# Kernel tuning notes

Hardware: AMD Instinct MI355X
Metric: run time of the kernel (lower is better)

Reference implementation:

```python
import jax, jax.numpy as jnp
import numpy as np

B = 32          # graphs per batch
NPG = 128       # nodes per graph
EPG = NPG * NPG # edges per graph (dense graph assumption in edge_delete_adap)
C = 64          # in_channels
EPS = 1e-6


def setup_inputs() -> dict:
    key = jax.random.key(0)
    k1, k2, k3, k4 = jax.random.split(key, 4)
    N = B * NPG
    x = jax.random.normal(k1, (N, C), jnp.float32)
    # dense per-graph edges, grouped contiguously by graph (required by the
    # reshape to [B, EPG] inside edge_delete_adap)
    a = jnp.arange(EPG, dtype=jnp.int32)
    src = a // NPG
    dst = a % NPG
    offs = (jnp.arange(B, dtype=jnp.int32) * NPG)[:, None]
    edge_index = jnp.stack([
        (src[None, :] + offs).reshape(-1),
        (dst[None, :] + offs).reshape(-1),
    ])  # [2, B*EPG] int32
    batch = jnp.repeat(jnp.arange(B, dtype=jnp.int32), NPG)  # node -> graph id
    W = jax.random.normal(k2, (2 * C, 1), jnp.float32) / np.sqrt(2 * C).astype(np.float32)
    b = jnp.zeros((1,), jnp.float32)
    rate1 = jax.random.uniform(k3, (B, EPG), jnp.float32)
    rate2 = jax.random.uniform(k4, (B, EPG), jnp.float32)
    return {"x": x, "edge_index": edge_index, "batch": batch,
            "W": W, "b": b, "rate1": rate1, "rate2": rate2}


def _edge_delete_adap(score_flat, rate, nodes):
    # score_flat: [B*EPG]; rate: [B, EPG]
    Bg, E = rate.shape
    s = score_flat.reshape(Bg, E)
    mn = jnp.min(s, axis=1, keepdims=True)
    mx = jnp.max(s, axis=1, keepdims=True)
    s = (s - mn) / (mx - mn + EPS)                  # per-graph min/max normalize
    mask = rate > (1.0 - s)                          # stochastic edge keep
    row = jnp.arange(Bg, dtype=jnp.int32)[:, None]
    col = jnp.arange(E, dtype=jnp.int32)[None, :]
    # index arithmetic from the original nonzero-based selection, computed for
    # ALL positions (padded form); mask marks which columns torch.nonzero keeps.
    idx0 = col // nodes + row * nodes
    idx1 = col % nodes + row * nodes
    new_edge_index = jnp.stack([idx0.reshape(-1), idx1.reshape(-1)])  # [2, B*E]
    return new_edge_index, mask.reshape(-1), s


def reference(x, edge_index, batch, W, b, rate1, rate2):
    # gather + concat edge endpoint features: [E_total, 2C] (dominant traffic)
    feat = jnp.concatenate([x[edge_index[0]], x[edge_index[1]]], axis=-1)
    raw = jax.nn.relu(feat @ W + b)                 # [E_total, 1]; dropout p=0.0
    score = jax.nn.sigmoid(raw).reshape(-1)         # [E_total]
    ei1, m1, s1 = _edge_delete_adap(score, rate1, NPG)
    ei2, m2, s2 = _edge_delete_adap(score, rate2, NPG)
    # original returns (new_edge_index1, new_edge_index2, batch, new_edge_score);
    # dynamic-shape nonzero outputs are returned in padded form + boolean mask.
    return ei1, m1, ei2, m2, batch, s1
```

## Files before the change

### kernel.cpp

```cpp
#include <hip/hip_runtime.h>
#include <math.h>

#define BGRAPH 32
#define NPG    128
#define EPG    (NPG * NPG)
#define CCH    64
#define ETOT   (BGRAPH * EPG)
#define NTOT   (BGRAPH * NPG)

__global__ __launch_bounds__(NPG) void node_kernel(
    const float* __restrict__ x,
    const float* __restrict__ W,
    const float* __restrict__ b,
    double* __restrict__ u,
    double* __restrict__ v,
    double* __restrict__ g_mn,
    double* __restrict__ g_den,
    float* __restrict__ out_batch)
{
    const int g = blockIdx.x;
    const int t = threadIdx.x;
    const int n = g * NPG + t;

    const float* xp = x + (size_t)n * CCH;
    double su = 0.0, sv = 0.0;
    #pragma unroll
    for (int c = 0; c < CCH; ++c) {
        double xc = (double)xp[c];
        su += xc * (double)W[c];
        sv += xc * (double)W[CCH + c];
    }
    const double uu = su + (double)b[0];
    u[n] = uu;
    v[n] = sv;
    out_batch[n] = (float)g;

    __shared__ double r0[NPG], r1[NPG], r2[NPG], r3[NPG];
    r0[t] = uu;
    r1[t] = uu;
    r2[t] = sv;
    r3[t] = sv;
    __syncthreads();
    for (int s = NPG / 2; s > 0; s >>= 1) {
        if (t < s) {
            r0[t] = fmin(r0[t], r0[t + s]);
            r1[t] = fmax(r1[t], r1[t + s]);
            r2[t] = fmin(r2[t], r2[t + s]);
            r3[t] = fmax(r3[t], r3[t + s]);
        }
        __syncthreads();
    }
    if (t == 0) {
        double tmin = r0[0] + r2[0];
        double tmax = r1[0] + r3[0];
        double rmin = tmin > 0.0 ? tmin : 0.0;
        double rmax = tmax > 0.0 ? tmax : 0.0;
        double smn = 1.0 / (1.0 + exp(-rmin));
        double smx = 1.0 / (1.0 + exp(-rmax));
        g_mn[g]  = smn;
        g_den[g] = smx - smn + 1e-6;
    }
}

__global__ __launch_bounds__(256) void edge_kernel(
    const double* __restrict__ u,
    const double* __restrict__ v,
    const double* __restrict__ g_mn,
    const double* __restrict__ g_den,
    const float* __restrict__ rate1,
    const float* __restrict__ rate2,
    float* __restrict__ out)
{
    const int tid = blockIdx.x * blockDim.x + threadIdx.x;
    const int idx = tid << 2;
    const int g   = idx >> 14;
    const int e   = idx & (EPG - 1);
    const int i   = e >> 7;
    const int j0  = e & 127;

    const double uu  = u[g * NPG + i];
    const double mn  = g_mn[g];
    const double den = g_den[g];
    const double* vp = v + g * NPG + j0;

    float4 r1 = *(const float4*)(rate1 + idx);
    float4 r2 = *(const float4*)(rate2 + idx);
    float r1a[4] = {r1.x, r1.y, r1.z, r1.w};
    float r2a[4] = {r2.x, r2.y, r2.z, r2.w};

    float sa[4], m1a[4], m2a[4], i1a[4];
    #pragma unroll
    for (int k = 0; k < 4; ++k) {
        double t   = uu + vp[k];
        double raw = t > 0.0 ? t : 0.0;
        double sig = 1.0 / (1.0 + exp(-raw));
        double s   = (sig - mn) / den;
        double thr = 1.0 - s;
        m1a[k] = ((double)r1a[k] > thr) ? 1.0f : 0.0f;
        m2a[k] = ((double)r2a[k] > thr) ? 1.0f : 0.0f;
        sa[k]  = (float)s;
        i1a[k] = (float)(j0 + k + g * NPG);
    }
    const float i0f = (float)(i + g * NPG);
    float4 i0v = make_float4(i0f, i0f, i0f, i0f);
    float4 i1v = make_float4(i1a[0], i1a[1], i1a[2], i1a[3]);
    float4 m1v = make_float4(m1a[0], m1a[1], m1a[2], m1a[3]);
    float4 m2v = make_float4(m2a[0], m2a[1], m2a[2], m2a[3]);
    float4 sv  = make_float4(sa[0],  sa[1],  sa[2],  sa[3]);

    *(float4*)(out + 0 * (size_t)ETOT + idx) = i0v;
    *(float4*)(out + 1 * (size_t)ETOT + idx) = i1v;
    *(float4*)(out + 2 * (size_t)ETOT + idx) = m1v;
    *(float4*)(out + 3 * (size_t)ETOT + idx) = i0v;
    *(float4*)(out + 4 * (size_t)ETOT + idx) = i1v;
    *(float4*)(out + 5 * (size_t)ETOT + idx) = m2v;
    *(float4*)(out + 6 * (size_t)ETOT + NTOT + idx) = sv;
}

extern "C" void kernel_launch(void* const* d_in, const int* in_sizes, int n_in,
                              void* d_out, int out_size, void* d_ws, size_t ws_size,
                              hipStream_t stream) {
    const float* x     = (const float*)d_in[0];
    const float* W     = (const float*)d_in[3];
    const float* b     = (const float*)d_in[4];
    const float* rate1 = (const float*)d_in[5];
    const float* rate2 = (const float*)d_in[6];
    float* out = (float*)d_out;

    double* u    = (double*)d_ws;
    double* v    = u + NTOT;
    double* gmn  = v + NTOT;
    double* gden = gmn + BGRAPH;

    float* out_batch = out + 6 * (size_t)ETOT;

    node_kernel<<<BGRAPH, NPG, 0, stream>>>(x, W, b, u, v, gmn, gden, out_batch);
    edge_kernel<<<ETOT / 4 / 256, 256, 0, stream>>>(u, v, gmn, gden, rate1, rate2, out);
}
```

Measured before the change: 78.34 us.

## Fuse node projection and edge scoring into one kernel with shared-memory node values

Merges the node and edge kernels into a single launch. Each of the 512 blocks recomputes its graph's node projections (u, v) and the per-graph min/max into shared memory, then scores its 1024 edges. This removes the second launch, the global-memory round trip for u/v/min/max, and the dependency between the two kernels. In exchange, each graph's node work is done 16 times redundantly, which adds x reads and a reduction before the edge work can start in every block. The x loads now use float4.

```diff
diff --git a/kernel.cpp b/kernel.cpp
--- a/kernel.cpp
+++ b/kernel.cpp
@@ -8,80 +8,80 @@
 #define ETOT   (BGRAPH * EPG)
 #define NTOT   (BGRAPH * NPG)
 
-__global__ __launch_bounds__(NPG) void node_kernel(
+__global__ __launch_bounds__(256) void fused_kernel(
     const float* __restrict__ x,
     const float* __restrict__ W,
     const float* __restrict__ b,
-    double* __restrict__ u,
-    double* __restrict__ v,
-    double* __restrict__ g_mn,
-    double* __restrict__ g_den,
-    float* __restrict__ out_batch)
+    const float* __restrict__ rate1,
+    const float* __restrict__ rate2,
+    float* __restrict__ out)
 {
-    const int g = blockIdx.x;
-    const int t = threadIdx.x;
-    const int n = g * NPG + t;
+    const int blk   = blockIdx.x;
+    const int t     = threadIdx.x;
+    const int g     = blk >> 4;
+    const int chunk = blk & 15;
 
-    const float* xp = x + (size_t)n * CCH;
-    double su = 0.0, sv = 0.0;
-    #pragma unroll
-    for (int c = 0; c < CCH; ++c) {
-        double xc = (double)xp[c];
-        su += xc * (double)W[c];
-        sv += xc * (double)W[CCH + c];
+    __shared__ double us[NPG], vs[NPG];
+    __shared__ double rmn0[NPG], rmx0[NPG], rmn1[NPG], rmx1[NPG];
+    __shared__ double s_mn, s_den;
+
+    if (t < NPG) {
+        const int n = g * NPG + t;
+        const float4* xp = (const float4*)(x + (size_t)n * CCH);
+        double su = 0.0, sv = 0.0;
+        #pragma unroll
+        for (int q = 0; q < CCH / 4; ++q) {
+            float4 xq = xp[q];
+            const int c = q * 4;
+            su += (double)xq.x * (double)W[c + 0];
+            su += (double)xq.y * (double)W[c + 1];
+            su += (double)xq.z * (double)W[c + 2];
+            su += (double)xq.w * (double)W[c + 3];
+            sv += (double)xq.x * (double)W[CCH + c + 0];
+            sv += (double)xq.y * (double)W[CCH + c + 1];
+            sv += (double)xq.z * (double)W[CCH + c + 2];
+            sv += (double)xq.w * (double)W[CCH + c + 3];
+        }
+        const double uu = su + (double)b[0];
+        us[t] = uu;  vs[t] = sv;
+        rmn0[t] = uu; rmx0[t] = uu;
+        rmn1[t] = sv; rmx1[t] = sv;
     }
-    const double uu = su + (double)b[0];
-    u[n] = uu;
-    v[n] = sv;
-    out_batch[n] = (float)g;
+    if (blk < 16) {
+        const int n = blk * 256 + t;
+        out[6 * (size_t)ETOT + n] = (float)(n >> 7);
+    }
+    __syncthreads();
 
-    __shared__ double r0[NPG], r1[NPG], r2[NPG], r3[NPG];
-    r0[t] = uu;
-    r1[t] = uu;
-    r2[t] = sv;
-    r3[t] = sv;
-    __syncthreads();
     for (int s = NPG / 2; s > 0; s >>= 1) {
         if (t < s) {
-            r0[t] = fmin(r0[t], r0[t + s]);
-            r1[t] = fmax(r1[t], r1[t + s]);
-            r2[t] = fmin(r2[t], r2[t + s]);
-            r3[t] = fmax(r3[t], r3[t + s]);
+            rmn0[t] = fmin(rmn0[t], rmn0[t + s]);
+            rmx0[t] = fmax(rmx0[t], rmx0[t + s]);
+            rmn1[t] = fmin(rmn1[t], rmn1[t + s]);
+            rmx1[t] = fmax(rmx1[t], rmx1[t + s]);
         }
         __syncthreads();
     }
     if (t == 0) {
-        double tmin = r0[0] + r2[0];
-        double tmax = r1[0] + r3[0];
+        double tmin = rmn0[0] + rmn1[0];
+        double tmax = rmx0[0] + rmx1[0];
         double rmin = tmin > 0.0 ? tmin : 0.0;
         double rmax = tmax > 0.0 ? tmax : 0.0;
         double smn = 1.0 / (1.0 + exp(-rmin));
         double smx = 1.0 / (1.0 + exp(-rmax));
-        g_mn[g]  = smn;
-        g_den[g] = smx - smn + 1e-6;
+        s_mn  = smn;
+        s_den = smx - smn + 1e-6;
     }
-}
+    __syncthreads();
 
-__global__ __launch_bounds__(256) void edge_kernel(
-    const double* __restrict__ u,
-    const double* __restrict__ v,
-    const double* __restrict__ g_mn,
-    const double* __restrict__ g_den,
-    const float* __restrict__ rate1,
-    const float* __restrict__ rate2,
-    float* __restrict__ out)
-{
-    const int tid = blockIdx.x * blockDim.x + threadIdx.x;
-    const int idx = tid << 2;
-    const int g   = idx >> 14;
-    const int e   = idx & (EPG - 1);
+    const int e   = chunk * 1024 + t * 4;
     const int i   = e >> 7;
     const int j0  = e & 127;
+    const int idx = g * EPG + e;
 
-    const double uu  = u[g * NPG + i];
-    const double mn  = g_mn[g];
-    const double den = g_den[g];
-    const double* vp = v + g * NPG + j0;
+    const double uu  = us[i];
+    const double mn  = s_mn;
+    const double den = s_den;
 
     float4 r1 = *(const float4*)(rate1 + idx);
     float4 r2 = *(const float4*)(rate2 + idx);
@@ -91,8 +91,8 @@
     float sa[4], m1a[4], m2a[4], i1a[4];
     #pragma unroll
     for (int k = 0; k < 4; ++k) {
-        double t   = uu + vp[k];
-        double raw = t > 0.0 ? t : 0.0;
+        double tt  = uu + vs[j0 + k];
+        double raw = tt > 0.0 ? tt : 0.0;
         double sig = 1.0 / (1.0 + exp(-raw));
         double s   = (sig - mn) / den;
         double thr = 1.0 - s;
@@ -127,13 +127,5 @@
     const float* rate2 = (const float*)d_in[6];
     float* out = (float*)d_out;
 
-    double* u    = (double*)d_ws;
-    double* v    = u + NTOT;
-    double* gmn  = v + NTOT;
-    double* gden = gmn + BGRAPH;
-
-    float* out_batch = out + 6 * (size_t)ETOT;
-
-    node_kernel<<<BGRAPH, NPG, 0, stream>>>(x, W, b, u, v, gmn, gden, out_batch);
-    edge_kernel<<<ETOT / 4 / 256, 256, 0, stream>>>(u, v, gmn, gden, rate1, rate2, out);
+    fused_kernel<<<BGRAPH * 16, 256, 0, stream>>>(x, W, b, rate1, rate2, out);
 }
```

New measurement: 78.22 us. No clear change (-0.2%).
